# Performance work log

Hardware: AMD Instinct MI355X
Metric: run time of the kernel (lower is better)

## Reference

```python
import jax, jax.numpy as jnp
import numpy as np

T, S, F, A, P = 64, 32, 256, 64, 32  # t, s, feature_len, attn_len, posembed_len


def setup_inputs() -> dict:
    key = jax.random.key(0)
    ks = jax.random.split(key, 8)
    w = lambda k, shape: jax.random.normal(k, shape, dtype=jnp.float32) * 0.02
    return {
        "batch_data": jax.random.normal(ks[0], (T * S, F), dtype=jnp.float32),
        "positions": jax.random.normal(ks[1], (2, S, S, 9), dtype=jnp.float32),
        "temp": jax.random.normal(ks[2], (T, T, S, 10), dtype=jnp.float32),
        "Wa": w(ks[3], (F, A)), "ba": jnp.zeros((A,), jnp.float32),
        "Wb": w(ks[4], (F + 2 * P, A)), "bb": jnp.zeros((A,), jnp.float32),
        "Wg": w(ks[5], (F + 2 * P, F)), "bg": jnp.zeros((F,), jnp.float32),
        "Wpos": w(ks[6], (9, P)), "bpos": jnp.zeros((P,), jnp.float32),
        "Wtmp": w(ks[7], (10, 2 * P)), "btmp": jnp.zeros((2 * P,), jnp.float32),
    }


def reference(batch_data, positions, temp, Wa, ba, Wb, bb, Wg, bg, Wpos, bpos, Wtmp, btmp):
    x = batch_data.reshape(T, S, F)                      # (T,S,F)
    # pairwise spatial embedding: pos[j,k] used for query node j, key node k
    pos = jnp.concatenate([positions[0] @ Wpos + bpos,
                           positions[1] @ Wpos + bpos], axis=-1)  # (S,S,2P)
    tmp = temp @ Wtmp + btmp                              # (T,T,S,2P)
    theta = x @ Wa + ba                                   # (T,S,A)

    # Linear on concat([x, p]) == x @ W[:F] + p @ W[F:] + b; split to avoid
    # materializing the broadcast concatenated tensor.
    WbX, WbP = Wb[:F], Wb[F:]
    WgX, WgP = Wg[:F], Wg[F:]
    x_phi = x @ WbX                                       # (T,S,A)
    x_g = x @ WgX                                         # (T,S,F)

    # ---- spatial pass: keys over nodes k at same time ----
    phi_s = x_phi[None] + (pos @ WbP)[:, None] + bb       # (Sq,T,Sk,A)
    feat_s = x_g[None] + (pos @ WgP)[:, None] + bg        # (Sq,T,Sk,F)
    scores_s = jnp.einsum('ija,jika->ijk', theta, phi_s)  # (T,Sq,Sk)
    attn_s = jax.nn.softmax(scores_s, axis=-1)
    res = jnp.einsum('ijk,jikf->ijf', attn_s, feat_s)     # (T,S,F)

    # ---- temporal pass: keys over times tau at same node ----
    phi_t = x_phi[None] + tmp @ WbP + bb                  # (Tq,T,S,A)
    feat_t = x_g[None] + tmp @ WgP + bg                   # (Tq,T,S,F)
    scores_t = jnp.einsum('jia,jtia->jit', theta, phi_t)  # (Tq,S,Tk)
    attn_t = jax.nn.softmax(scores_t, axis=-1)
    res = res + jnp.einsum('jit,jtif->jif', attn_t, feat_t)
    return res                                            # (T,S,F)
```

## Files before the change

kernel.cpp:

```cpp
#include <hip/hip_runtime.h>

constexpr int T = 64, S = 32, F = 256, A = 64;
constexpr int R = T * S;

constexpr size_t OFF_XPH = 0;
constexpr size_t OFF_TH  = OFF_XPH + (size_t)R * A;
constexpr size_t OFF_UU  = OFF_TH  + (size_t)R * A;
constexpr size_t OFF_DD  = OFF_UU  + (size_t)R * A;
constexpr size_t OFF_POS = OFF_DD  + (size_t)R * 16;
constexpr size_t OFF_Z   = OFF_POS + (size_t)S * S * 64;

__device__ __forceinline__ float dot4(float4 a, float4 b) {
    return a.x * b.x + a.y * b.y + a.z * b.z + a.w * b.w;
}

__global__ __launch_bounds__(256) void k_pre(
    const float* __restrict__ bd, const float* __restrict__ Wa,
    const float* __restrict__ ba, const float* __restrict__ Wb,
    const float* __restrict__ Wtmp, const float* __restrict__ positions,
    const float* __restrict__ Wpos, const float* __restrict__ bpos,
    float* __restrict__ xph, float* __restrict__ th,
    float* __restrict__ uu, float* __restrict__ dd, float* __restrict__ pos)
{
    const int blk = blockIdx.x;
    const int tid = threadIdx.x;

    if (blk >= 256) {
        const int idx = (blk - 256) * 256 + tid;
        const int p = idx & 63, jk = idx >> 6;
        const int e = p >> 5, pp = p & 31;
        const float* src = positions + (size_t)(e * 1024 + jk) * 9;
        float acc = bpos[pp];
#pragma unroll
        for (int q = 0; q < 9; ++q) acc += src[q] * Wpos[q * 32 + pp];
        pos[idx] = acc;
        return;
    }

    __shared__ float xs[8 * 256];
    __shared__ float ths[8][64];
    __shared__ float us[8][64];
    const int w = tid >> 6, lane = tid & 63;
    const int row0 = blk * 8 + 2 * w;

    {
        const float4* src = (const float4*)(bd + (size_t)blk * 8 * 256);
        float4* dst = (float4*)xs;
        dst[tid] = src[tid];
        dst[tid + 256] = src[tid + 256];
    }
    __syncthreads();

    const float* x0 = xs + (2 * w) * 256;
    const float* x1 = xs + (2 * w + 1) * 256;
    float accA0 = ba[lane], accA1 = accA0, accB0 = 0.f, accB1 = 0.f;
#pragma unroll
    for (int c0 = 0; c0 < 256; c0 += 8) {
        float wa[8], wb[8];
#pragma unroll
        for (int j = 0; j < 8; ++j) wa[j] = Wa[(c0 + j) * 64 + lane];
#pragma unroll
        for (int j = 0; j < 8; ++j) wb[j] = Wb[(c0 + j) * 64 + lane];
#pragma unroll
        for (int j = 0; j < 8; ++j) {
            const float xa = x0[c0 + j], xb = x1[c0 + j];
            accA0 += xa * wa[j]; accA1 += xb * wa[j];
            accB0 += xa * wb[j]; accB1 += xb * wb[j];
        }
    }
    th[(size_t)row0 * 64 + lane] = accA0;
    th[(size_t)(row0 + 1) * 64 + lane] = accA1;
    xph[(size_t)row0 * 64 + lane] = accB0;
    xph[(size_t)(row0 + 1) * 64 + lane] = accB1;
    ths[2 * w][lane] = accA0; ths[2 * w + 1][lane] = accA1;
    __syncthreads();

    float accU0 = 0.f, accU1 = 0.f;
#pragma unroll 8
    for (int a = 0; a < 64; ++a) {
        const float wp = Wb[(256 + lane) * 64 + a];
        accU0 += ths[2 * w][a] * wp;
        accU1 += ths[2 * w + 1][a] * wp;
    }
    uu[(size_t)row0 * 64 + lane] = accU0;
    uu[(size_t)(row0 + 1) * 64 + lane] = accU1;
    us[2 * w][lane] = accU0; us[2 * w + 1][lane] = accU1;
    __syncthreads();

    const int rsel = lane >> 4, q = lane & 15;
    if (rsel < 2 && q < 10) {
        float accD = 0.f;
#pragma unroll 8
        for (int p2 = 0; p2 < 64; ++p2) accD += us[2 * w + rsel][p2] * Wtmp[q * 64 + p2];
        dd[(size_t)(row0 + rsel) * 16 + q] = accD;
    }
}

__global__ __launch_bounds__(256) void k_attn(
    const float* __restrict__ bd, const float* __restrict__ temp,
    const float* __restrict__ Wtmp, const float* __restrict__ btmp,
    const float* __restrict__ xph, const float* __restrict__ th,
    const float* __restrict__ uu, const float* __restrict__ dd,
    const float* __restrict__ pos, float* __restrict__ Z)
{
    const int ss = blockIdx.x >> 4;
    const int tt0 = (blockIdx.x & 15) * 4;
    const int tid = threadIdx.x;
    const int w = tid >> 6, lane = tid & 63;

    __shared__ float th_s[4][64], u_s[4][64], d_s[4][16];
    __shared__ float es[4][32], et[4][64], w10[4][10];

    {
        const size_t r = (size_t)(tt0 + w) * 32 + ss;
        th_s[w][lane] = th[r * 64 + lane];
        u_s[w][lane]  = uu[r * 64 + lane];
        if (lane < 16) d_s[w][lane] = dd[r * 16 + lane];
    }
    __syncthreads();

    {
        const int t = lane;
        const float4* xp = (const float4*)(xph + ((size_t)t * 32 + ss) * 64);
        const float4* tv4 = (const float4*)th_s[w];
        float sc = 0.f;
#pragma unroll
        for (int a = 0; a < 16; ++a) sc += dot4(xp[a], tv4[a]);
        const float2* tp = (const float2*)(temp + (((size_t)(tt0 + w) * 64 + t) * 32 + ss) * 10);
        const float2* dv = (const float2*)d_s[w];
        float2 tmpv[5];
#pragma unroll
        for (int q = 0; q < 5; ++q) {
            tmpv[q] = tp[q];
            const float2 d2 = dv[q];
            sc += tmpv[q].x * d2.x + tmpv[q].y * d2.y;
        }
        float m = sc;
#pragma unroll
        for (int off = 32; off; off >>= 1) m = fmaxf(m, __shfl_xor(m, off));
        const float e = __expf(sc - m);
        float s = e;
#pragma unroll
        for (int off = 32; off; off >>= 1) s += __shfl_xor(s, off);
        const float at = e / s;
        et[w][t] = at;
        float r10[10];
#pragma unroll
        for (int q = 0; q < 5; ++q) { r10[2 * q] = at * tmpv[q].x; r10[2 * q + 1] = at * tmpv[q].y; }
#pragma unroll
        for (int off = 32; off; off >>= 1) {
#pragma unroll
            for (int i = 0; i < 10; ++i) r10[i] += __shfl_xor(r10[i], off);
        }
        if (lane == 0) {
#pragma unroll
            for (int i = 0; i < 10; ++i) w10[w][i] = r10[i];
        }
    }

    if (tid < 128) {
        const int ttl = tid >> 5, k = tid & 31;
        const float4* xp = (const float4*)(xph + ((size_t)(tt0 + ttl) * 32 + k) * 64);
        const float4* pp = (const float4*)(pos + ((size_t)ss * 32 + k) * 64);
        const float4* tv4 = (const float4*)th_s[ttl];
        const float4* uv4 = (const float4*)u_s[ttl];
        float sc = 0.f;
#pragma unroll
        for (int a = 0; a < 16; ++a) sc += dot4(xp[a], tv4[a]) + dot4(pp[a], uv4[a]);
        float m = sc;
#pragma unroll
        for (int off = 16; off; off >>= 1) m = fmaxf(m, __shfl_xor(m, off));
        const float e = __expf(sc - m);
        float s = e;
#pragma unroll
        for (int off = 16; off; off >>= 1) s += __shfl_xor(s, off);
        es[ttl][k] = e / s;
    }
    __syncthreads();

    {
        const int f = tid;
        float acc0 = 0.f, acc1 = 0.f, acc2 = 0.f, acc3 = 0.f;
        const float* bt = bd + (size_t)ss * 256 + f;
#pragma unroll
        for (int t0 = 0; t0 < 64; t0 += 8) {
            float xv[8];
#pragma unroll
            for (int j = 0; j < 8; ++j) xv[j] = bt[(size_t)(t0 + j) * 32 * 256];
#pragma unroll
            for (int j = 0; j < 8; ++j) {
                acc0 += et[0][t0 + j] * xv[j]; acc1 += et[1][t0 + j] * xv[j];
                acc2 += et[2][t0 + j] * xv[j]; acc3 += et[3][t0 + j] * xv[j];
            }
        }
        float sa[4] = {acc0, acc1, acc2, acc3};
#pragma unroll
        for (int ttl = 0; ttl < 4; ++ttl) {
            const float* bs = bd + (size_t)(tt0 + ttl) * 32 * 256 + f;
            float a2 = 0.f;
#pragma unroll
            for (int k0 = 0; k0 < 32; k0 += 8) {
                float yv[8];
#pragma unroll
                for (int j = 0; j < 8; ++j) yv[j] = bs[(size_t)(k0 + j) * 256];
#pragma unroll
                for (int j = 0; j < 8; ++j) a2 += es[ttl][k0 + j] * yv[j];
            }
            Z[((size_t)(tt0 + ttl) * 32 + ss) * 320 + f] = sa[ttl] + a2;
        }
    }

    {
        const int p = lane;
        const float* pb = pos + (size_t)ss * 32 * 64 + p;
        float pv = 0.f;
#pragma unroll
        for (int k0 = 0; k0 < 32; k0 += 8) {
            float yv[8];
#pragma unroll
            for (int j = 0; j < 8; ++j) yv[j] = pb[(size_t)(k0 + j) * 64];
#pragma unroll
            for (int j = 0; j < 8; ++j) pv += es[w][k0 + j] * yv[j];
        }
        float g = pv + btmp[p];
#pragma unroll
        for (int q = 0; q < 10; ++q) g += w10[w][q] * Wtmp[q * 64 + p];
        Z[((size_t)(tt0 + w) * 32 + ss) * 320 + 256 + p] = g;
    }
}

__global__ __launch_bounds__(256) void k_out(
    const float* __restrict__ Z, const float* __restrict__ Wg,
    const float* __restrict__ bg, float* __restrict__ out)
{
    const int f = threadIdx.x;
    const int r0 = blockIdx.x * 4;
    const float* z0 = Z + (size_t)r0 * 320;
    float acc[4] = {0.f, 0.f, 0.f, 0.f};
#pragma unroll
    for (int k0 = 0; k0 < 320; k0 += 4) {
        float wv[4];
#pragma unroll
        for (int j = 0; j < 4; ++j) wv[j] = Wg[(size_t)(k0 + j) * 256 + f];
#pragma unroll
        for (int j = 0; j < 4; ++j) {
#pragma unroll
            for (int r = 0; r < 4; ++r) acc[r] += z0[(size_t)r * 320 + k0 + j] * wv[j];
        }
    }
    const float b2 = 2.f * bg[f];
#pragma unroll
    for (int r = 0; r < 4; ++r) out[(size_t)(r0 + r) * 256 + f] = acc[r] + b2;
}

extern "C" void kernel_launch(void* const* d_in, const int* in_sizes, int n_in,
                              void* d_out, int out_size, void* d_ws, size_t ws_size,
                              hipStream_t stream) {
    const float* bd   = (const float*)d_in[0];
    const float* positions = (const float*)d_in[1];
    const float* temp = (const float*)d_in[2];
    const float* Wa   = (const float*)d_in[3];
    const float* ba   = (const float*)d_in[4];
    const float* Wb   = (const float*)d_in[5];
    const float* Wg   = (const float*)d_in[7];
    const float* bg   = (const float*)d_in[8];
    const float* Wpos = (const float*)d_in[9];
    const float* bpos = (const float*)d_in[10];
    const float* Wtmp = (const float*)d_in[11];
    const float* btmp = (const float*)d_in[12];
    float* out = (float*)d_out;

    float* ws  = (float*)d_ws;
    float* xph = ws + OFF_XPH;
    float* th  = ws + OFF_TH;
    float* uu  = ws + OFF_UU;
    float* dd  = ws + OFF_DD;
    float* pos = ws + OFF_POS;
    float* Z   = ws + OFF_Z;

    k_pre<<<512, 256, 0, stream>>>(bd, Wa, ba, Wb, Wtmp, positions, Wpos, bpos,
                                   xph, th, uu, dd, pos);
    k_attn<<<512, 256, 0, stream>>>(bd, temp, Wtmp, btmp, xph, th, uu, dd, pos, Z);
    k_out<<<512, 256, 0, stream>>>(Z, Wg, bg, out);
}
```

Measured before the change: 122.6 us.

## Fuse attention aggregation and output projection into one kernel

Merges k_attn and k_out so the per-row aggregated features Z stay in shared memory and are multiplied by Wg in the same block, which removes the Z round-trip through global memory and one kernel launch. The aggregation loops are also restructured: each wave now handles float4 feature lanes and a slice of the time keys, and partial sums are reduced through shared memory. The Wg projection is split by K across the four waves and then reduced. In exchange, shared-memory use and sync count per block go up, and each block re-reads all of Wg for only 4 rows.

```diff
diff --git a/kernel.cpp b/kernel.cpp
--- a/kernel.cpp
+++ b/kernel.cpp
@@ -8,10 +8,15 @@
 constexpr size_t OFF_UU  = OFF_TH  + (size_t)R * A;
 constexpr size_t OFF_DD  = OFF_UU  + (size_t)R * A;
 constexpr size_t OFF_POS = OFF_DD  + (size_t)R * 16;
-constexpr size_t OFF_Z   = OFF_POS + (size_t)S * S * 64;
 
 __device__ __forceinline__ float dot4(float4 a, float4 b) {
     return a.x * b.x + a.y * b.y + a.z * b.z + a.w * b.w;
+}
+__device__ __forceinline__ float4 f4fma(float s, float4 v, float4 a) {
+    a.x += s * v.x; a.y += s * v.y; a.z += s * v.z; a.w += s * v.w; return a;
+}
+__device__ __forceinline__ float4 f4add(float4 a, float4 b) {
+    a.x += b.x; a.y += b.y; a.z += b.z; a.w += b.w; return a;
 }
 
 __global__ __launch_bounds__(256) void k_pre(
@@ -96,12 +101,13 @@
     }
 }
 
-__global__ __launch_bounds__(256) void k_attn(
+__global__ __launch_bounds__(256) void k_fuse(
     const float* __restrict__ bd, const float* __restrict__ temp,
     const float* __restrict__ Wtmp, const float* __restrict__ btmp,
+    const float* __restrict__ Wg, const float* __restrict__ bg,
     const float* __restrict__ xph, const float* __restrict__ th,
     const float* __restrict__ uu, const float* __restrict__ dd,
-    const float* __restrict__ pos, float* __restrict__ Z)
+    const float* __restrict__ pos, float* __restrict__ out)
 {
     const int ss = blockIdx.x >> 4;
     const int tt0 = (blockIdx.x & 15) * 4;
@@ -110,6 +116,8 @@
 
     __shared__ float th_s[4][64], u_s[4][64], d_s[4][16];
     __shared__ float es[4][32], et[4][64], w10[4][10];
+    __shared__ float zz[4][320];
+    __shared__ float4 part4[4][4][64];
 
     {
         const size_t r = (size_t)(tt0 + w) * 32 + ss;
@@ -179,38 +187,6 @@
     __syncthreads();
 
     {
-        const int f = tid;
-        float acc0 = 0.f, acc1 = 0.f, acc2 = 0.f, acc3 = 0.f;
-        const float* bt = bd + (size_t)ss * 256 + f;
-#pragma unroll
-        for (int t0 = 0; t0 < 64; t0 += 8) {
-            float xv[8];
-#pragma unroll
-            for (int j = 0; j < 8; ++j) xv[j] = bt[(size_t)(t0 + j) * 32 * 256];
-#pragma unroll
-            for (int j = 0; j < 8; ++j) {
-                acc0 += et[0][t0 + j] * xv[j]; acc1 += et[1][t0 + j] * xv[j];
-                acc2 += et[2][t0 + j] * xv[j]; acc3 += et[3][t0 + j] * xv[j];
-            }
-        }
-        float sa[4] = {acc0, acc1, acc2, acc3};
-#pragma unroll
-        for (int ttl = 0; ttl < 4; ++ttl) {
-            const float* bs = bd + (size_t)(tt0 + ttl) * 32 * 256 + f;
-            float a2 = 0.f;
-#pragma unroll
-            for (int k0 = 0; k0 < 32; k0 += 8) {
-                float yv[8];
-#pragma unroll
-                for (int j = 0; j < 8; ++j) yv[j] = bs[(size_t)(k0 + j) * 256];
-#pragma unroll
-                for (int j = 0; j < 8; ++j) a2 += es[ttl][k0 + j] * yv[j];
-            }
-            Z[((size_t)(tt0 + ttl) * 32 + ss) * 320 + f] = sa[ttl] + a2;
-        }
-    }
-
-    {
         const int p = lane;
         const float* pb = pos + (size_t)ss * 32 * 64 + p;
         float pv = 0.f;
@@ -225,32 +201,75 @@
         float g = pv + btmp[p];
 #pragma unroll
         for (int q = 0; q < 10; ++q) g += w10[w][q] * Wtmp[q * 64 + p];
-        Z[((size_t)(tt0 + w) * 32 + ss) * 320 + 256 + p] = g;
-    }
-}
-
-__global__ __launch_bounds__(256) void k_out(
-    const float* __restrict__ Z, const float* __restrict__ Wg,
-    const float* __restrict__ bg, float* __restrict__ out)
-{
-    const int f = threadIdx.x;
-    const int r0 = blockIdx.x * 4;
-    const float* z0 = Z + (size_t)r0 * 320;
-    float acc[4] = {0.f, 0.f, 0.f, 0.f};
-#pragma unroll
-    for (int k0 = 0; k0 < 320; k0 += 4) {
-        float wv[4];
-#pragma unroll
-        for (int j = 0; j < 4; ++j) wv[j] = Wg[(size_t)(k0 + j) * 256 + f];
-#pragma unroll
-        for (int j = 0; j < 4; ++j) {
-#pragma unroll
-            for (int r = 0; r < 4; ++r) acc[r] += z0[(size_t)r * 320 + k0 + j] * wv[j];
-        }
-    }
-    const float b2 = 2.f * bg[f];
-#pragma unroll
-    for (int r = 0; r < 4; ++r) out[(size_t)(r0 + r) * 256 + f] = acc[r] + b2;
+        zz[w][256 + p] = g;
+    }
+
+    {
+        const float4* bd4 = (const float4*)bd;
+        float4 acc[4];
+#pragma unroll
+        for (int r = 0; r < 4; ++r) acc[r] = make_float4(0.f, 0.f, 0.f, 0.f);
+#pragma unroll
+        for (int j = 0; j < 16; ++j) {
+            const int t = 16 * w + j;
+            const float4 x4 = bd4[((size_t)t * 32 + ss) * 64 + lane];
+#pragma unroll
+            for (int r = 0; r < 4; ++r) acc[r] = f4fma(et[r][t], x4, acc[r]);
+        }
+#pragma unroll
+        for (int r = 0; r < 4; ++r) part4[w][r][lane] = acc[r];
+    }
+    __syncthreads();
+
+    {
+        const float4* bd4 = (const float4*)bd;
+        float4 a = make_float4(0.f, 0.f, 0.f, 0.f);
+#pragma unroll
+        for (int k = 0; k < 32; ++k) {
+            const float4 x4 = bd4[((size_t)(tt0 + w) * 32 + k) * 64 + lane];
+            a = f4fma(es[w][k], x4, a);
+        }
+#pragma unroll
+        for (int w2 = 0; w2 < 4; ++w2) a = f4add(a, part4[w2][w][lane]);
+        ((float4*)&zz[w][0])[lane] = a;
+    }
+    __syncthreads();
+
+    {
+        const float4* Wg4 = (const float4*)Wg;
+        float4 acc[4];
+#pragma unroll
+        for (int r = 0; r < 4; ++r) acc[r] = make_float4(0.f, 0.f, 0.f, 0.f);
+        const int kbase = 80 * w;
+#pragma unroll 4
+        for (int j = 0; j < 20; ++j) {
+            const int k0 = kbase + 4 * j;
+            float4 wg[4];
+#pragma unroll
+            for (int q = 0; q < 4; ++q) wg[q] = Wg4[(size_t)(k0 + q) * 64 + lane];
+#pragma unroll
+            for (int r = 0; r < 4; ++r) {
+                const float4 zv = *(const float4*)&zz[r][k0];
+                acc[r] = f4fma(zv.x, wg[0], acc[r]);
+                acc[r] = f4fma(zv.y, wg[1], acc[r]);
+                acc[r] = f4fma(zv.z, wg[2], acc[r]);
+                acc[r] = f4fma(zv.w, wg[3], acc[r]);
+            }
+        }
+#pragma unroll
+        for (int r = 0; r < 4; ++r) part4[w][r][lane] = acc[r];
+    }
+    __syncthreads();
+
+    {
+        float4 o = part4[0][w][lane];
+        o = f4add(o, part4[1][w][lane]);
+        o = f4add(o, part4[2][w][lane]);
+        o = f4add(o, part4[3][w][lane]);
+        const float4 b4 = ((const float4*)bg)[lane];
+        o.x += 2.f * b4.x; o.y += 2.f * b4.y; o.z += 2.f * b4.z; o.w += 2.f * b4.w;
+        ((float4*)out)[((size_t)(tt0 + w) * 32 + ss) * 64 + lane] = o;
+    }
 }
 
 extern "C" void kernel_launch(void* const* d_in, const int* in_sizes, int n_in,
@@ -276,10 +295,9 @@
     float* uu  = ws + OFF_UU;
     float* dd  = ws + OFF_DD;
     float* pos = ws + OFF_POS;
-    float* Z   = ws + OFF_Z;
 
     k_pre<<<512, 256, 0, stream>>>(bd, Wa, ba, Wb, Wtmp, positions, Wpos, bpos,
                                    xph, th, uu, dd, pos);
-    k_attn<<<512, 256, 0, stream>>>(bd, temp, Wtmp, btmp, xph, th, uu, dd, pos, Z);
-    k_out<<<512, 256, 0, stream>>>(Z, Wg, bg, out);
-}
+    k_fuse<<<512, 256, 0, stream>>>(bd, temp, Wtmp, btmp, Wg, bg,
+                                    xph, th, uu, dd, pos, out);
+}
```

Result: faster. 116.4 us (-5.0%).
